# Optimization experiments

Hardware: AMD Instinct MI355X
Metric: run time of the kernel (lower is better)

## Reference

```python
import jax, jax.numpy as jnp
import numpy as np

N = 40000
E = 640000
D_IN = 128
D_OUT = 128
K = 3
LAMBDA_MAX = 2.0
LN_EPS = 1e-5


def setup_inputs() -> dict:
    key = jax.random.key(0)
    k1, k2, k3, k4, k5 = jax.random.split(key, 5)
    x = jax.random.normal(k1, (N, D_IN), dtype=jnp.float32)
    edge_index = jax.random.randint(k2, (2, E), 0, N, dtype=jnp.int64)
    edge_weight = jax.random.uniform(k3, (E,), dtype=jnp.float32)
    # Chebyshev weights: one [D_IN, D_OUT] matrix per hop k, plus shared bias
    W = jax.random.normal(k4, (K, D_IN, D_OUT), dtype=jnp.float32) / np.sqrt(D_IN)
    bias = jnp.zeros((D_OUT,), dtype=jnp.float32)
    gamma = jnp.ones((D_OUT,), dtype=jnp.float32)
    beta = jnp.zeros((D_OUT,), dtype=jnp.float32)
    return {"x": x, "edge_weight": edge_weight, "W": W, "bias": bias,
            "gamma": gamma, "beta": beta, "edge_index": edge_index}


def reference(x, edge_weight, W, bias, gamma, beta, edge_index):
    row, col = edge_index[0], edge_index[1]

    # Symmetric normalization of the graph Laplacian (PyG ChebConv, norm='sym')
    deg = jax.ops.segment_sum(edge_weight, row, num_segments=N)
    dinv = jnp.where(deg > 0, jax.lax.rsqrt(deg), 0.0)
    # scaled Laplacian L_hat = (2/lambda_max) * (I - A_norm) - I
    # off-diagonal entries: -(2/lambda_max) * a_norm ; diagonal: 2/lambda_max - 1
    scale = 2.0 / LAMBDA_MAX
    norm = -scale * dinv[row] * edge_weight * dinv[col]  # [E]
    diag = scale - 1.0  # == 0 for lambda_max = 2

    def prop(h):  # L_hat @ h via gather / scale / scatter-add
        msg = norm[:, None] * h[col]                      # [E, D]
        return jax.ops.segment_sum(msg, row, num_segments=N) + diag * h

    # Chebyshev recursion: T0 = x, T1 = L_hat x, Tk = 2 L_hat T_{k-1} - T_{k-2}
    Tx0 = x
    out = Tx0 @ W[0]
    Tx1 = prop(x)
    out = out + Tx1 @ W[1]
    for k in range(2, K):
        Tx2 = 2.0 * prop(Tx1) - Tx0
        out = out + Tx2 @ W[k]
        Tx0, Tx1 = Tx1, Tx2
    out = out + bias

    # LayerNorm over channels + ReLU
    mean = jnp.mean(out, axis=-1, keepdims=True)
    var = jnp.var(out, axis=-1, keepdims=True)
    out = (out - mean) * jax.lax.rsqrt(var + LN_EPS) * gamma + beta
    return jax.nn.relu(out)
```

## Files before the change

### kernel.cpp

```cpp
#include <hip/hip_runtime.h>

#define NN 40000
#define EE 640000
#define DD 128
#define CAP 96

typedef __attribute__((ext_vector_type(8))) __bf16 bf16x8;
typedef __attribute__((ext_vector_type(4))) float f32x4;
typedef unsigned long long ull;

static __device__ __forceinline__ unsigned short bfs(float f) {
    __bf16 h = (__bf16)f;
    return __builtin_bit_cast(unsigned short, h);
}
static __device__ __forceinline__ float blo(unsigned int v) {
    return __builtin_bit_cast(float, v << 16);
}
static __device__ __forceinline__ float bhi(unsigned int v) {
    return __builtin_bit_cast(float, v & 0xffff0000u);
}
static __device__ __forceinline__ float dinv_of(ull dc) {
    unsigned int lo = (unsigned int)dc;
    return lo > 0 ? rsqrtf((float)lo * (1.0f / 16777216.0f)) : 0.0f;
}

__global__ __launch_bounds__(256) void k_pre(const int* __restrict__ ei,
                                             const float* __restrict__ ew,
                                             const float* __restrict__ x,
                                             const float* __restrict__ W,
                                             ull* __restrict__ degcnt,
                                             int2* __restrict__ pair,
                                             unsigned short* __restrict__ xb,
                                             unsigned short* __restrict__ Wt) {
    int b = blockIdx.x;
    int tid = threadIdx.x;
    if (b < 2500) {
        int e = b * 256 + tid;
        int r = ei[e];
        int c = ei[EE + e];
        float w = ew[e];
        unsigned int q = __float2uint_rn(w * 16777216.0f);
        ull old = atomicAdd(degcnt + r, (1ULL << 32) | (ull)q);
        int rk = (int)(old >> 32);
        if (rk < CAP)
            pair[(size_t)r * CAP + rk] = make_int2(c, __float_as_int(w));
    } else if (b < 3125) {
        int base = (b - 2500) * 2048 + tid;
        #pragma unroll
        for (int it = 0; it < 8; it++) {
            int i = base + it * 256;
            float4 v = ((const float4*)x)[i];
            ushort4 p;
            p.x = bfs(v.x); p.y = bfs(v.y); p.z = bfs(v.z); p.w = bfs(v.w);
            ((ushort4*)xb)[i] = p;
        }
    } else {
        int t = (b - 3125) * 256 + tid;
        int n = t / 384;
        int c = t - n * 384;
        Wt[t] = bfs(W[(size_t)c * 128 + n]);
    }
}

__global__ __launch_bounds__(256) void k_prop(const ull* __restrict__ degcnt,
                                              const int2* __restrict__ pair,
                                              const unsigned short* __restrict__ hb,
                                              const unsigned short* __restrict__ subb,
                                              float alpha, float betac,
                                              unsigned short* __restrict__ outb) {
    int grp = (blockIdx.x * 256 + threadIdx.x) >> 4;
    int q = threadIdx.x & 15;

    ull dc = degcnt[grp];
    int cnt = (int)(dc >> 32);
    if (cnt > CAP) cnt = CAP;
    float dr = dinv_of(dc);

    int s = grp * CAP, t = s + cnt;
    float a0 = 0.f, a1 = 0.f, a2 = 0.f, a3 = 0.f, a4 = 0.f, a5 = 0.f, a6 = 0.f, a7 = 0.f;

    int e = s;
    for (; e + 4 <= t; e += 4) {
        int2 p0 = pair[e + 0];
        int2 p1 = pair[e + 1];
        int2 p2 = pair[e + 2];
        int2 p3 = pair[e + 3];
        uint4 h0 = *(const uint4*)(hb + (size_t)p0.x * DD + q * 8);
        uint4 h1 = *(const uint4*)(hb + (size_t)p1.x * DD + q * 8);
        uint4 h2 = *(const uint4*)(hb + (size_t)p2.x * DD + q * 8);
        uint4 h3 = *(const uint4*)(hb + (size_t)p3.x * DD + q * 8);
        float n0 = __int_as_float(p0.y) * dinv_of(degcnt[p0.x]);
        float n1 = __int_as_float(p1.y) * dinv_of(degcnt[p1.x]);
        float n2 = __int_as_float(p2.y) * dinv_of(degcnt[p2.x]);
        float n3 = __int_as_float(p3.y) * dinv_of(degcnt[p3.x]);
        a0 = fmaf(n0, blo(h0.x), a0); a1 = fmaf(n0, bhi(h0.x), a1);
        a2 = fmaf(n0, blo(h0.y), a2); a3 = fmaf(n0, bhi(h0.y), a3);
        a4 = fmaf(n0, blo(h0.z), a4); a5 = fmaf(n0, bhi(h0.z), a5);
        a6 = fmaf(n0, blo(h0.w), a6); a7 = fmaf(n0, bhi(h0.w), a7);
        a0 = fmaf(n1, blo(h1.x), a0); a1 = fmaf(n1, bhi(h1.x), a1);
        a2 = fmaf(n1, blo(h1.y), a2); a3 = fmaf(n1, bhi(h1.y), a3);
        a4 = fmaf(n1, blo(h1.z), a4); a5 = fmaf(n1, bhi(h1.z), a5);
        a6 = fmaf(n1, blo(h1.w), a6); a7 = fmaf(n1, bhi(h1.w), a7);
        a0 = fmaf(n2, blo(h2.x), a0); a1 = fmaf(n2, bhi(h2.x), a1);
        a2 = fmaf(n2, blo(h2.y), a2); a3 = fmaf(n2, bhi(h2.y), a3);
        a4 = fmaf(n2, blo(h2.z), a4); a5 = fmaf(n2, bhi(h2.z), a5);
        a6 = fmaf(n2, blo(h2.w), a6); a7 = fmaf(n2, bhi(h2.w), a7);
        a0 = fmaf(n3, blo(h3.x), a0); a1 = fmaf(n3, bhi(h3.x), a1);
        a2 = fmaf(n3, blo(h3.y), a2); a3 = fmaf(n3, bhi(h3.y), a3);
        a4 = fmaf(n3, blo(h3.z), a4); a5 = fmaf(n3, bhi(h3.z), a5);
        a6 = fmaf(n3, blo(h3.w), a6); a7 = fmaf(n3, bhi(h3.w), a7);
    }
    if (e < t) {
        int i1 = (e + 1 < t) ? e + 1 : t - 1;
        int i2 = (e + 2 < t) ? e + 2 : t - 1;
        float m1 = (e + 1 < t) ? 1.f : 0.f;
        float m2 = (e + 2 < t) ? 1.f : 0.f;
        int2 p0 = pair[e];
        int2 p1 = pair[i1];
        int2 p2 = pair[i2];
        uint4 h0 = *(const uint4*)(hb + (size_t)p0.x * DD + q * 8);
        uint4 h1 = *(const uint4*)(hb + (size_t)p1.x * DD + q * 8);
        uint4 h2 = *(const uint4*)(hb + (size_t)p2.x * DD + q * 8);
        float n0 = __int_as_float(p0.y) * dinv_of(degcnt[p0.x]);
        float n1 = m1 * __int_as_float(p1.y) * dinv_of(degcnt[p1.x]);
        float n2 = m2 * __int_as_float(p2.y) * dinv_of(degcnt[p2.x]);
        a0 = fmaf(n0, blo(h0.x), a0); a1 = fmaf(n0, bhi(h0.x), a1);
        a2 = fmaf(n0, blo(h0.y), a2); a3 = fmaf(n0, bhi(h0.y), a3);
        a4 = fmaf(n0, blo(h0.z), a4); a5 = fmaf(n0, bhi(h0.z), a5);
        a6 = fmaf(n0, blo(h0.w), a6); a7 = fmaf(n0, bhi(h0.w), a7);
        a0 = fmaf(n1, blo(h1.x), a0); a1 = fmaf(n1, bhi(h1.x), a1);
        a2 = fmaf(n1, blo(h1.y), a2); a3 = fmaf(n1, bhi(h1.y), a3);
        a4 = fmaf(n1, blo(h1.z), a4); a5 = fmaf(n1, bhi(h1.z), a5);
        a6 = fmaf(n1, blo(h1.w), a6); a7 = fmaf(n1, bhi(h1.w), a7);
        a0 = fmaf(n2, blo(h2.x), a0); a1 = fmaf(n2, bhi(h2.x), a1);
        a2 = fmaf(n2, blo(h2.y), a2); a3 = fmaf(n2, bhi(h2.y), a3);
        a4 = fmaf(n2, blo(h2.z), a4); a5 = fmaf(n2, bhi(h2.z), a5);
        a6 = fmaf(n2, blo(h2.w), a6); a7 = fmaf(n2, bhi(h2.w), a7);
    }

    float scale = -alpha * dr;
    if (subb != nullptr) {
        const unsigned short* sp = subb + (size_t)grp * DD + q * 8;
        uint4 sv = *(const uint4*)sp;
        a0 = fmaf(scale, a0, betac * blo(sv.x));
        a1 = fmaf(scale, a1, betac * bhi(sv.x));
        a2 = fmaf(scale, a2, betac * blo(sv.y));
        a3 = fmaf(scale, a3, betac * bhi(sv.y));
        a4 = fmaf(scale, a4, betac * blo(sv.z));
        a5 = fmaf(scale, a5, betac * bhi(sv.z));
        a6 = fmaf(scale, a6, betac * blo(sv.w));
        a7 = fmaf(scale, a7, betac * bhi(sv.w));
    } else {
        a0 *= scale; a1 *= scale; a2 *= scale; a3 *= scale;
        a4 *= scale; a5 *= scale; a6 *= scale; a7 *= scale;
    }
    ushort4 o0, o1;
    o0.x = bfs(a0); o0.y = bfs(a1); o0.z = bfs(a2); o0.w = bfs(a3);
    o1.x = bfs(a4); o1.y = bfs(a5); o1.z = bfs(a6); o1.w = bfs(a7);
    unsigned short* op = outb + (size_t)grp * DD + q * 8;
    *(ushort4*)(op) = o0;
    *(ushort4*)(op + 4) = o1;
}

__global__ __launch_bounds__(320) void k_gemm_mfma_ln(
        const unsigned short* __restrict__ xb, const unsigned short* __restrict__ t1b,
        const unsigned short* __restrict__ t2b, const unsigned short* __restrict__ Wt,
        const float* __restrict__ bias, const float* __restrict__ gamma,
        const float* __restrict__ beta, float* __restrict__ out) {
    int tid = threadIdx.x;
    int lane = tid & 63;
    int wv = tid >> 6;
    int quad = lane >> 4;
    int l15 = lane & 15;
    int rowq = blockIdx.x * 160 + wv * 32;

    int r0 = rowq + l15;
    int r1 = rowq + 16 + l15;

    float bias_l[8], gamma_l[8], beta_l[8];
    #pragma unroll
    for (int nt = 0; nt < 8; nt++) {
        int cc = nt * 16 + l15;
        bias_l[nt] = bias[cc];
        gamma_l[nt] = gamma[cc];
        beta_l[nt] = beta[cc];
    }

    f32x4 acc[2][8];
    #pragma unroll
    for (int mt = 0; mt < 2; mt++)
        #pragma unroll
        for (int nt = 0; nt < 8; nt++)
            acc[mt][nt] = (f32x4){0.f, 0.f, 0.f, 0.f};

    #pragma unroll
    for (int c = 0; c < 12; c++) {
        const unsigned short* src = (c < 4) ? xb : ((c < 8) ? t1b : t2b);
        int kk = (c & 3) * 32 + quad * 8;
        bf16x8 a0 = *(const bf16x8*)(src + (size_t)r0 * DD + kk);
        bf16x8 a1 = *(const bf16x8*)(src + (size_t)r1 * DD + kk);
        #pragma unroll
        for (int nt = 0; nt < 8; nt++) {
            bf16x8 b = *(const bf16x8*)(Wt + (size_t)(nt * 16 + l15) * 384 + c * 32 + quad * 8);
            acc[0][nt] = __builtin_amdgcn_mfma_f32_16x16x32_bf16(a0, b, acc[0][nt], 0, 0, 0);
            acc[1][nt] = __builtin_amdgcn_mfma_f32_16x16x32_bf16(a1, b, acc[1][nt], 0, 0, 0);
        }
    }

    #pragma unroll
    for (int mt = 0; mt < 2; mt++) {
        #pragma unroll
        for (int reg = 0; reg < 4; reg++) {
            float v[8];
            float s = 0.f, sq = 0.f;
            #pragma unroll
            for (int nt = 0; nt < 8; nt++) {
                v[nt] = acc[mt][nt][reg] + bias_l[nt];
                s += v[nt];
                sq += v[nt] * v[nt];
            }
            #pragma unroll
            for (int m = 1; m <= 8; m <<= 1) {
                s  += __shfl_xor(s, m, 64);
                sq += __shfl_xor(sq, m, 64);
            }
            float mean = s * (1.0f / 128.0f);
            float var = sq * (1.0f / 128.0f) - mean * mean;
            float inv = rsqrtf(var + 1e-5f);
            int grow = rowq + mt * 16 + quad * 4 + reg;
            #pragma unroll
            for (int nt = 0; nt < 8; nt++) {
                float o = fmaxf((v[nt] - mean) * inv * gamma_l[nt] + beta_l[nt], 0.0f);
                out[(size_t)grow * DD + nt * 16 + l15] = o;
            }
        }
    }
}

extern "C" void kernel_launch(void* const* d_in, const int* in_sizes, int n_in,
                              void* d_out, int out_size, void* d_ws, size_t ws_size,
                              hipStream_t stream) {
    const float* x     = (const float*)d_in[0];
    const float* ew    = (const float*)d_in[1];
    const float* W     = (const float*)d_in[2];
    const float* bias  = (const float*)d_in[3];
    const float* gamma = (const float*)d_in[4];
    const float* beta  = (const float*)d_in[5];
    const int*   ei    = (const int*)d_in[6];
    float* out = (float*)d_out;

    char* ws = (char*)d_ws;
    size_t o = 0;
    auto alloc = [&](size_t bytes) { void* p = ws + o; o += (bytes + 255) & ~(size_t)255; return p; };
    ull*   degcnt = (ull*) alloc((size_t)NN * 8);
    int2*  pair  = (int2*) alloc((size_t)NN * CAP * 8);
    unsigned short* xb  = (unsigned short*)alloc((size_t)NN * DD * 2);
    unsigned short* t1b = (unsigned short*)alloc((size_t)NN * DD * 2);
    unsigned short* t2b = (unsigned short*)alloc((size_t)NN * DD * 2);
    unsigned short* Wt  = (unsigned short*)alloc((size_t)384 * 128 * 2);

    hipMemsetAsync(degcnt, 0, (size_t)NN * 8, stream);

    k_pre<<<3317, 256, 0, stream>>>(ei, ew, x, W, degcnt, pair, xb, Wt);

    k_prop<<<NN / 16, 256, 0, stream>>>(degcnt, pair, xb, nullptr, 1.0f, 0.0f, t1b);
    k_prop<<<NN / 16, 256, 0, stream>>>(degcnt, pair, t1b, xb, 2.0f, -1.0f, t2b);

    k_gemm_mfma_ln<<<250, 320, 0, stream>>>(xb, t1b, t2b, Wt, bias, gamma, beta, out);
}
```

Measured before the change: 212.8 us.

## Pack degree and count into 32-bit atomics, precompute dinv, prefetch edge pairs

Degree and per-row edge count now share one 32-bit word (8-bit count, 24-bit fixed-point weight sum) instead of a 64-bit word. That makes the atomics and the per-neighbour gathers narrower. A new small kernel computes dinv once per node, so the propagation loop gathers a float instead of recomputing rsqrt for every edge. The edge-pair loads for the next group of four are issued before the current accumulation to hide latency. The costs are an extra kernel launch, lower fixed-point precision for the degree sum, and an overflow risk if any node has more than 255 edges.

```diff
diff --git a/kernel.cpp b/kernel.cpp
--- a/kernel.cpp
+++ b/kernel.cpp
@@ -7,7 +7,6 @@
 
 typedef __attribute__((ext_vector_type(8))) __bf16 bf16x8;
 typedef __attribute__((ext_vector_type(4))) float f32x4;
-typedef unsigned long long ull;
 
 static __device__ __forceinline__ unsigned short bfs(float f) {
     __bf16 h = (__bf16)f;
@@ -18,17 +17,13 @@
 }
 static __device__ __forceinline__ float bhi(unsigned int v) {
     return __builtin_bit_cast(float, v & 0xffff0000u);
-}
-static __device__ __forceinline__ float dinv_of(ull dc) {
-    unsigned int lo = (unsigned int)dc;
-    return lo > 0 ? rsqrtf((float)lo * (1.0f / 16777216.0f)) : 0.0f;
 }
 
 __global__ __launch_bounds__(256) void k_pre(const int* __restrict__ ei,
                                              const float* __restrict__ ew,
                                              const float* __restrict__ x,
                                              const float* __restrict__ W,
-                                             ull* __restrict__ degcnt,
+                                             unsigned int* __restrict__ degcnt,
                                              int2* __restrict__ pair,
                                              unsigned short* __restrict__ xb,
                                              unsigned short* __restrict__ Wt) {
@@ -39,9 +34,9 @@
         int r = ei[e];
         int c = ei[EE + e];
         float w = ew[e];
-        unsigned int q = __float2uint_rn(w * 16777216.0f);
-        ull old = atomicAdd(degcnt + r, (1ULL << 32) | (ull)q);
-        int rk = (int)(old >> 32);
+        unsigned int q = __float2uint_rn(w * 65536.0f);
+        unsigned int old = atomicAdd(degcnt + r, (1u << 24) | q);
+        int rk = (int)(old >> 24);
         if (rk < CAP)
             pair[(size_t)r * CAP + rk] = make_int2(c, __float_as_int(w));
     } else if (b < 3125) {
@@ -62,37 +57,49 @@
     }
 }
 
-__global__ __launch_bounds__(256) void k_prop(const ull* __restrict__ degcnt,
+__global__ __launch_bounds__(256) void k_dinv(const unsigned int* __restrict__ degcnt,
+                                              float* __restrict__ dinv) {
+    int i = blockIdx.x * 256 + threadIdx.x;
+    if (i < NN) {
+        unsigned int lo = degcnt[i] & 0x00ffffffu;
+        dinv[i] = lo > 0 ? rsqrtf((float)lo * (1.0f / 65536.0f)) : 0.0f;
+    }
+}
+
+__global__ __launch_bounds__(256) void k_prop(const unsigned int* __restrict__ degcnt,
                                               const int2* __restrict__ pair,
                                               const unsigned short* __restrict__ hb,
+                                              const float* __restrict__ dinv,
                                               const unsigned short* __restrict__ subb,
                                               float alpha, float betac,
                                               unsigned short* __restrict__ outb) {
     int grp = (blockIdx.x * 256 + threadIdx.x) >> 4;
     int q = threadIdx.x & 15;
 
-    ull dc = degcnt[grp];
-    int cnt = (int)(dc >> 32);
+    int cnt = (int)(degcnt[grp] >> 24);
     if (cnt > CAP) cnt = CAP;
-    float dr = dinv_of(dc);
+    float dr = dinv[grp];
 
     int s = grp * CAP, t = s + cnt;
     float a0 = 0.f, a1 = 0.f, a2 = 0.f, a3 = 0.f, a4 = 0.f, a5 = 0.f, a6 = 0.f, a7 = 0.f;
 
     int e = s;
-    for (; e + 4 <= t; e += 4) {
-        int2 p0 = pair[e + 0];
-        int2 p1 = pair[e + 1];
-        int2 p2 = pair[e + 2];
-        int2 p3 = pair[e + 3];
+    int2 p0, p1, p2, p3;
+    bool have = (e + 4 <= t);
+    if (have) { p0 = pair[e]; p1 = pair[e + 1]; p2 = pair[e + 2]; p3 = pair[e + 3]; }
+    while (have) {
         uint4 h0 = *(const uint4*)(hb + (size_t)p0.x * DD + q * 8);
         uint4 h1 = *(const uint4*)(hb + (size_t)p1.x * DD + q * 8);
         uint4 h2 = *(const uint4*)(hb + (size_t)p2.x * DD + q * 8);
         uint4 h3 = *(const uint4*)(hb + (size_t)p3.x * DD + q * 8);
-        float n0 = __int_as_float(p0.y) * dinv_of(degcnt[p0.x]);
-        float n1 = __int_as_float(p1.y) * dinv_of(degcnt[p1.x]);
-        float n2 = __int_as_float(p2.y) * dinv_of(degcnt[p2.x]);
-        float n3 = __int_as_float(p3.y) * dinv_of(degcnt[p3.x]);
+        float n0 = __int_as_float(p0.y) * dinv[p0.x];
+        float n1 = __int_as_float(p1.y) * dinv[p1.x];
+        float n2 = __int_as_float(p2.y) * dinv[p2.x];
+        float n3 = __int_as_float(p3.y) * dinv[p3.x];
+        int en = e + 4;
+        have = (en + 4 <= t);
+        if (have) { p0 = pair[en]; p1 = pair[en + 1]; p2 = pair[en + 2]; p3 = pair[en + 3]; }
+        e = en;
         a0 = fmaf(n0, blo(h0.x), a0); a1 = fmaf(n0, bhi(h0.x), a1);
         a2 = fmaf(n0, blo(h0.y), a2); a3 = fmaf(n0, bhi(h0.y), a3);
         a4 = fmaf(n0, blo(h0.z), a4); a5 = fmaf(n0, bhi(h0.z), a5);
@@ -115,15 +122,15 @@
         int i2 = (e + 2 < t) ? e + 2 : t - 1;
         float m1 = (e + 1 < t) ? 1.f : 0.f;
         float m2 = (e + 2 < t) ? 1.f : 0.f;
-        int2 p0 = pair[e];
-        int2 p1 = pair[i1];
-        int2 p2 = pair[i2];
-        uint4 h0 = *(const uint4*)(hb + (size_t)p0.x * DD + q * 8);
-        uint4 h1 = *(const uint4*)(hb + (size_t)p1.x * DD + q * 8);
-        uint4 h2 = *(const uint4*)(hb + (size_t)p2.x * DD + q * 8);
-        float n0 = __int_as_float(p0.y) * dinv_of(degcnt[p0.x]);
-        float n1 = m1 * __int_as_float(p1.y) * dinv_of(degcnt[p1.x]);
-        float n2 = m2 * __int_as_float(p2.y) * dinv_of(degcnt[p2.x]);
+        int2 q0 = pair[e];
+        int2 q1 = pair[i1];
+        int2 q2 = pair[i2];
+        uint4 h0 = *(const uint4*)(hb + (size_t)q0.x * DD + q * 8);
+        uint4 h1 = *(const uint4*)(hb + (size_t)q1.x * DD + q * 8);
+        uint4 h2 = *(const uint4*)(hb + (size_t)q2.x * DD + q * 8);
+        float n0 = __int_as_float(q0.y) * dinv[q0.x];
+        float n1 = m1 * __int_as_float(q1.y) * dinv[q1.x];
+        float n2 = m2 * __int_as_float(q2.y) * dinv[q2.x];
         a0 = fmaf(n0, blo(h0.x), a0); a1 = fmaf(n0, bhi(h0.x), a1);
         a2 = fmaf(n0, blo(h0.y), a2); a3 = fmaf(n0, bhi(h0.y), a3);
         a4 = fmaf(n0, blo(h0.z), a4); a5 = fmaf(n0, bhi(h0.z), a5);
@@ -252,19 +259,21 @@
     char* ws = (char*)d_ws;
     size_t o = 0;
     auto alloc = [&](size_t bytes) { void* p = ws + o; o += (bytes + 255) & ~(size_t)255; return p; };
-    ull*   degcnt = (ull*) alloc((size_t)NN * 8);
+    unsigned int* degcnt = (unsigned int*)alloc((size_t)NN * 4);
+    float* dinv  = (float*)alloc((size_t)NN * 4);
     int2*  pair  = (int2*) alloc((size_t)NN * CAP * 8);
     unsigned short* xb  = (unsigned short*)alloc((size_t)NN * DD * 2);
     unsigned short* t1b = (unsigned short*)alloc((size_t)NN * DD * 2);
     unsigned short* t2b = (unsigned short*)alloc((size_t)NN * DD * 2);
     unsigned short* Wt  = (unsigned short*)alloc((size_t)384 * 128 * 2);
 
-    hipMemsetAsync(degcnt, 0, (size_t)NN * 8, stream);
+    hipMemsetAsync(degcnt, 0, (size_t)NN * 4, stream);
 
     k_pre<<<3317, 256, 0, stream>>>(ei, ew, x, W, degcnt, pair, xb, Wt);
-
-    k_prop<<<NN / 16, 256, 0, stream>>>(degcnt, pair, xb, nullptr, 1.0f, 0.0f, t1b);
-    k_prop<<<NN / 16, 256, 0, stream>>>(degcnt, pair, t1b, xb, 2.0f, -1.0f, t2b);
+    k_dinv<<<(NN + 255) / 256, 256, 0, stream>>>(degcnt, dinv);
+
+    k_prop<<<NN / 16, 256, 0, stream>>>(degcnt, pair, xb, dinv, nullptr, 1.0f, 0.0f, t1b);
+    k_prop<<<NN / 16, 256, 0, stream>>>(degcnt, pair, t1b, dinv, xb, 2.0f, -1.0f, t2b);
 
     k_gemm_mfma_ln<<<250, 320, 0, stream>>>(xb, t1b, t2b, Wt, bias, gamma, beta, out);
 }
```

Result: faster. 193.3 us (median of 2 runs) (-9.1%).
